# Kernel optimization log

Hardware: AMD Instinct MI355X
Metric: run time of the kernel (lower is better)

Reference implementation:

```python
import jax, jax.numpy as jnp
import numpy as np

N = 256
FEAT = 1024           # box_head.fc7.out_features
HID_REL = 256         # RelationProposalNetwork hidden_dim
GCN_HID = 256         # gcn_hidden
HEADS = 4
NUM_PARTS = 20
OUT = NUM_PARTS + 1
TOPK = 3
IN_GCN = FEAT + 4


def setup_inputs() -> dict:
    key = jax.random.key(0)
    ks = jax.random.split(key, 16)
    features = jax.random.normal(ks[0], (N, FEAT), jnp.float32)
    # valid pixel-space boxes (x1, y1, x2, y2) inside an 800x800 image
    xy = jax.random.uniform(ks[1], (N, 2), jnp.float32, 0.0, 700.0)
    wh = jax.random.uniform(ks[2], (N, 2), jnp.float32, 8.0, 100.0)
    boxes = jnp.concatenate([xy, xy + wh], axis=1)
    s = 0.02
    W_fc1 = jax.random.normal(ks[3], (2 * FEAT + 4, HID_REL), jnp.float32) * s
    b_fc1 = jnp.zeros((HID_REL,), jnp.float32)
    W_fc2 = jax.random.normal(ks[4], (HID_REL, 1), jnp.float32) * s
    b_fc2 = jnp.zeros((1,), jnp.float32)
    W1 = jax.random.normal(ks[5], (IN_GCN, HEADS * GCN_HID), jnp.float32) * s
    a_src1 = jax.random.normal(ks[6], (HEADS, GCN_HID), jnp.float32) * s
    a_dst1 = jax.random.normal(ks[7], (HEADS, GCN_HID), jnp.float32) * s
    b1 = jnp.zeros((HEADS * GCN_HID,), jnp.float32)
    W2 = jax.random.normal(ks[8], (HEADS * GCN_HID, OUT), jnp.float32) * s
    a_src2 = jax.random.normal(ks[9], (1, OUT), jnp.float32) * s
    a_dst2 = jax.random.normal(ks[10], (1, OUT), jnp.float32) * s
    b2 = jnp.zeros((OUT,), jnp.float32)
    return {
        "features": features, "boxes": boxes,
        "W_fc1": W_fc1, "b_fc1": b_fc1, "W_fc2": W_fc2, "b_fc2": b_fc2,
        "W1": W1, "a_src1": a_src1, "a_dst1": a_dst1, "b1": b1,
        "W2": W2, "a_src2": a_src2, "a_dst2": a_dst2, "b2": b2,
        "img_h": 800, "img_w": 800,
    }


def _gat_layer(x, W, a_src, a_dst, bias, s, t, n, heads, ch):
    # PyG GATConv: message flows edge_index[0] (s) -> edge_index[1] (t),
    # softmax over incoming edges of each target node t.
    h = (x @ W).reshape(n, heads, ch)                       # [n, H, C]
    e = jax.nn.leaky_relu(
        jnp.einsum("ehc,hc->eh", h[s], a_src)
        + jnp.einsum("ehc,hc->eh", h[t], a_dst), 0.2)        # [E, H]
    m = jnp.full((n, heads), -1e30, e.dtype).at[t].max(e)    # segment max
    p = jnp.exp(e - m[t])
    denom = jax.ops.segment_sum(p, t, num_segments=n)
    alpha = p / denom[t]                                     # [E, H]
    out = jax.ops.segment_sum(alpha[:, :, None] * h[s], t, num_segments=n)
    return out.reshape(n, heads * ch) + bias


def _forward(features, boxes, W_fc1, b_fc1, W_fc2, b_fc2,
             W1, a_src1, a_dst1, b1, W2, a_src2, a_dst2, b2, img_h, img_w):
    n = features.shape[0]
    # --- RelationProposalNetwork: dense O(N^2) pairwise MLP ---
    f1 = jnp.broadcast_to(features[:, None, :], (n, n, FEAT))
    f2 = jnp.broadcast_to(features[None, :, :], (n, n, FEAT))
    geom = jnp.abs(boxes[:, None, :] - boxes[None, :, :])    # [n, n, 4]
    pair = jnp.concatenate([f1, f2, geom], axis=-1)          # [n, n, 2052]
    hid = jax.nn.relu(pair @ W_fc1 + b_fc1)                  # [n, n, 256]
    rel = (hid @ W_fc2 + b_fc2)[..., 0]                      # [n, n]
    # --- top-k graph construction (drop first = self, as in source) ---
    idx = jax.lax.top_k(rel, TOPK + 1)[1][:, 1:]             # [n, topk]
    s_e = jnp.repeat(jnp.arange(n), TOPK)                    # edge_index[0]
    t_e = idx.reshape(-1)                                    # edge_index[1]
    loops = jnp.arange(n)                                    # GATConv add_self_loops
    s_e = jnp.concatenate([s_e, loops])
    t_e = jnp.concatenate([t_e, loops])
    # --- normalized box geometry node features ---
    scale = jnp.array([img_w, img_h, img_w, img_h], jnp.float32)
    nb = boxes / scale
    geomn = jnp.stack([nb[:, 0], nb[:, 1], nb[:, 2] - nb[:, 0], nb[:, 3] - nb[:, 1]], axis=1)
    gcn_in = jnp.concatenate([features, geomn], axis=1)      # [n, 1028]
    # --- AttentionalGCN: GAT(heads=4) -> ReLU -> GAT(heads=1) ---
    h1 = jax.nn.relu(_gat_layer(gcn_in, W1, a_src1, a_dst1, b1, s_e, t_e, n, HEADS, GCN_HID))
    logits = _gat_layer(h1, W2, a_src2, a_dst2, b2, s_e, t_e, n, 1, OUT)
    return logits


def reference(features, boxes, W_fc1, b_fc1, W_fc2, b_fc2,
              W1, a_src1, a_dst1, b1, W2, a_src2, a_dst2, b2, img_h, img_w):
    logits = _forward(features, boxes, W_fc1, b_fc1, W_fc2, b_fc2,
                      W1, a_src1, a_dst1, b1, W2, a_src2, a_dst2, b2, img_h, img_w)
    labels = jnp.argmax(logits, axis=1)
    return logits, labels
```

## Files before the change

kernel.cpp:

```cpp
#include <hip/hip_runtime.h>
#include <math.h>

#define NN 256
#define FEAT 1024
#define HIDR 256
#define HEADS 4
#define GCNH 256
#define M1 1024
#define OUTC 21
#define MAXDEG (NN + 1)
#define KC 8
#define KCH (FEAT / KC)
#define FCOLS 1536

__global__ __launch_bounds__(256) void k_big(
        const float* __restrict__ feat, const float* __restrict__ Wfc1,
        const float* __restrict__ W1, float* __restrict__ P) {
    __shared__ float fS[8][KCH];
    int rg = blockIdx.x, cg = blockIdx.y, kc = blockIdx.z;
    int tid = threadIdx.x;
    int r0 = rg * 8, k0 = kc * KCH;
    for (int x = tid; x < 8 * KCH; x += 256) {
        int r = x >> 7, kk = x & (KCH - 1);
        fS[r][kk] = feat[(size_t)(r0 + r) * FEAT + k0 + kk];
    }
    __syncthreads();
    int gc = cg * 512 + tid * 2;
    const float* pW;
    int ld;
    if (gc < 256)      { pW = Wfc1 + (size_t)k0 * HIDR + gc;                  ld = HIDR; }
    else if (gc < 512) { pW = Wfc1 + (size_t)(FEAT + k0) * HIDR + (gc - 256); ld = HIDR; }
    else               { pW = W1   + (size_t)k0 * M1 + (gc - 512);            ld = M1;   }
    float2 acc[8];
#pragma unroll
    for (int r = 0; r < 8; r++) { acc[r].x = 0.f; acc[r].y = 0.f; }
    for (int kk = 0; kk < KCH; kk += 4) {
        float2 w0 = *(const float2*)(pW);
        float2 w1 = *(const float2*)(pW + ld);
        float2 w2 = *(const float2*)(pW + 2 * ld);
        float2 w3 = *(const float2*)(pW + 3 * ld);
        pW += 4 * ld;
#pragma unroll
        for (int r = 0; r < 8; r++) {
            float4 f = *(const float4*)&fS[r][kk];
            acc[r].x = fmaf(f.x, w0.x, acc[r].x); acc[r].y = fmaf(f.x, w0.y, acc[r].y);
            acc[r].x = fmaf(f.y, w1.x, acc[r].x); acc[r].y = fmaf(f.y, w1.y, acc[r].y);
            acc[r].x = fmaf(f.z, w2.x, acc[r].x); acc[r].y = fmaf(f.z, w2.y, acc[r].y);
            acc[r].x = fmaf(f.w, w3.x, acc[r].x); acc[r].y = fmaf(f.w, w3.y, acc[r].y);
        }
    }
    float* Pp = P + ((size_t)kc * NN + r0) * FCOLS + gc;
#pragma unroll
    for (int r = 0; r < 8; r++)
        *(float2*)(Pp + (size_t)r * FCOLS) = acc[r];
}

__global__ __launch_bounds__(384) void k_redfix(
        const float* __restrict__ P, const float* __restrict__ bfc1,
        const float* __restrict__ boxes, const int* __restrict__ imh,
        const int* __restrict__ imw, const float* __restrict__ W1,
        const float* __restrict__ as1, const float* __restrict__ ad1,
        float* __restrict__ A, float* __restrict__ BT,
        float* __restrict__ hpre, float* __restrict__ es1,
        float* __restrict__ ed1, float* __restrict__ geomn) {
    __shared__ float gS[4];
    int row = blockIdx.x, tid = threadIdx.x;
    int c4 = tid * 4;
    const float* p = P + (size_t)row * FCOLS + c4;
    const size_t str = (size_t)NN * FCOLS;
    float4 t0 = *(const float4*)(p);
    float4 t1 = *(const float4*)(p + str);
    float4 t2 = *(const float4*)(p + 2 * str);
    float4 t3 = *(const float4*)(p + 3 * str);
    float4 t4 = *(const float4*)(p + 4 * str);
    float4 t5 = *(const float4*)(p + 5 * str);
    float4 t6 = *(const float4*)(p + 6 * str);
    float4 t7 = *(const float4*)(p + 7 * str);
    float4 s;
    s.x = ((t0.x + t1.x) + (t2.x + t3.x)) + ((t4.x + t5.x) + (t6.x + t7.x));
    s.y = ((t0.y + t1.y) + (t2.y + t3.y)) + ((t4.y + t5.y) + (t6.y + t7.y));
    s.z = ((t0.z + t1.z) + (t2.z + t3.z)) + ((t4.z + t5.z) + (t6.z + t7.z));
    s.w = ((t0.w + t1.w) + (t2.w + t3.w)) + ((t4.w + t5.w) + (t6.w + t7.w));
    if (tid == 0) {
        float w = (float)imw[0], h = (float)imh[0];
        float x1 = boxes[row * 4 + 0] / w, y1 = boxes[row * 4 + 1] / h;
        float x2 = boxes[row * 4 + 2] / w, y2 = boxes[row * 4 + 3] / h;
        gS[0] = x1; gS[1] = y1; gS[2] = x2 - x1; gS[3] = y2 - y1;
        geomn[row * 4 + 0] = x1;
        geomn[row * 4 + 1] = y1;
        geomn[row * 4 + 2] = x2 - x1;
        geomn[row * 4 + 3] = y2 - y1;
    }
    __syncthreads();
    if (c4 < 256) {
        float4 b = *(const float4*)(bfc1 + c4);
        s.x += b.x; s.y += b.y; s.z += b.z; s.w += b.w;
        *(float4*)(A + (size_t)row * HIDR + c4) = s;
    } else if (c4 < 512) {
        int kk = c4 - 256;
        BT[(kk + 0) * NN + row] = s.x;
        BT[(kk + 1) * NN + row] = s.y;
        BT[(kk + 2) * NN + row] = s.z;
        BT[(kk + 3) * NN + row] = s.w;
    } else {
        int ch = c4 - 512;
        float g0 = gS[0], g1 = gS[1], g2 = gS[2], g3 = gS[3];
        float4 wv;
        wv = *(const float4*)(W1 + (size_t)(FEAT + 0) * M1 + ch);
        s.x = fmaf(g0, wv.x, s.x); s.y = fmaf(g0, wv.y, s.y);
        s.z = fmaf(g0, wv.z, s.z); s.w = fmaf(g0, wv.w, s.w);
        wv = *(const float4*)(W1 + (size_t)(FEAT + 1) * M1 + ch);
        s.x = fmaf(g1, wv.x, s.x); s.y = fmaf(g1, wv.y, s.y);
        s.z = fmaf(g1, wv.z, s.z); s.w = fmaf(g1, wv.w, s.w);
        wv = *(const float4*)(W1 + (size_t)(FEAT + 2) * M1 + ch);
        s.x = fmaf(g2, wv.x, s.x); s.y = fmaf(g2, wv.y, s.y);
        s.z = fmaf(g2, wv.z, s.z); s.w = fmaf(g2, wv.w, s.w);
        wv = *(const float4*)(W1 + (size_t)(FEAT + 3) * M1 + ch);
        s.x = fmaf(g3, wv.x, s.x); s.y = fmaf(g3, wv.y, s.y);
        s.z = fmaf(g3, wv.z, s.z); s.w = fmaf(g3, wv.w, s.w);
        *(float4*)(hpre + (size_t)row * M1 + ch) = s;
        float4 a = *(const float4*)(as1 + ch);
        float4 b = *(const float4*)(ad1 + ch);
        float ps = s.x * a.x + s.y * a.y + s.z * a.z + s.w * a.w;
        float pd = s.x * b.x + s.y * b.y + s.z * b.z + s.w * b.w;
#pragma unroll
        for (int o = 32; o > 0; o >>= 1) {
            ps += __shfl_down(ps, o);
            pd += __shfl_down(pd, o);
        }
        if ((tid & 63) == 0) {
            int head = (tid - 128) >> 6;
            es1[row * 4 + head] = ps;
            ed1[row * 4 + head] = pd;
        }
    }
}

__global__ __launch_bounds__(512) void k_reltopk(
        const float* __restrict__ A, const float* __restrict__ BT,
        const float* __restrict__ boxes, const float* __restrict__ Wfc1,
        const float* __restrict__ Wfc2, int* __restrict__ idxTop) {
    __shared__ float As[HIDR], w2s[HIDR], wg0[HIDR], wg1[HIDR], wg2[HIDR], wg3[HIDR];
    __shared__ float sval[512];
    __shared__ unsigned long long swk[8];
    __shared__ int win;
    int i = blockIdx.x, tid = threadIdx.x;
    int j = tid & 255, half = tid >> 8;
    if (tid < 256) {
        As[tid]  = A[i * HIDR + tid];
        w2s[tid] = Wfc2[tid];
        wg0[tid] = Wfc1[(size_t)(2 * FEAT + 0) * HIDR + tid];
    } else {
        int q = tid - 256;
        wg1[q] = Wfc1[(size_t)(2 * FEAT + 1) * HIDR + q];
        wg2[q] = Wfc1[(size_t)(2 * FEAT + 2) * HIDR + q];
        wg3[q] = Wfc1[(size_t)(2 * FEAT + 3) * HIDR + q];
    }
    float bi0 = boxes[i * 4 + 0], bi1 = boxes[i * 4 + 1];
    float bi2 = boxes[i * 4 + 2], bi3 = boxes[i * 4 + 3];
    float g0 = fabsf(bi0 - boxes[j * 4 + 0]);
    float g1 = fabsf(bi1 - boxes[j * 4 + 1]);
    float g2 = fabsf(bi2 - boxes[j * 4 + 2]);
    float g3 = fabsf(bi3 - boxes[j * 4 + 3]);
    __syncthreads();
    int k0 = half * 128;
    const float* pB = BT + (size_t)k0 * NN + j;
    float acc = 0.f;
    for (int kk = k0; kk < k0 + 128; kk += 4) {
        float4 a4 = *(const float4*)&As[kk];
        float4 w4 = *(const float4*)&w2s[kk];
        float4 q0 = *(const float4*)&wg0[kk];
        float4 q1 = *(const float4*)&wg1[kk];
        float4 q2 = *(const float4*)&wg2[kk];
        float4 q3 = *(const float4*)&wg3[kk];
        float b0 = pB[0], b1 = pB[NN], b2 = pB[2 * NN], b3 = pB[3 * NN];
        pB += 4 * NN;
        float v;
        v = a4.x + b0; v = fmaf(g0, q0.x, v); v = fmaf(g1, q1.x, v);
        v = fmaf(g2, q2.x, v); v = fmaf(g3, q3.x, v);
        acc = fmaf(fmaxf(v, 0.f), w4.x, acc);
        v = a4.y + b1; v = fmaf(g0, q0.y, v); v = fmaf(g1, q1.y, v);
        v = fmaf(g2, q2.y, v); v = fmaf(g3, q3.y, v);
        acc = fmaf(fmaxf(v, 0.f), w4.y, acc);
        v = a4.z + b2; v = fmaf(g0, q0.z, v); v = fmaf(g1, q1.z, v);
        v = fmaf(g2, q2.z, v); v = fmaf(g3, q3.z, v);
        acc = fmaf(fmaxf(v, 0.f), w4.z, acc);
        v = a4.w + b3; v = fmaf(g0, q0.w, v); v = fmaf(g1, q1.w, v);
        v = fmaf(g2, q2.w, v); v = fmaf(g3, q3.w, v);
        acc = fmaf(fmaxf(v, 0.f), w4.w, acc);
    }
    sval[tid] = acc;
    __syncthreads();
    if (tid < 256) sval[tid] = sval[tid] + sval[tid + 256];
    __syncthreads();
    for (int r = 0; r < 4; r++) {
        unsigned long long key = 0ULL;
        if (tid < 256) {
            unsigned u = __float_as_uint(sval[tid]);
            u = (u & 0x80000000u) ? ~u : (u | 0x80000000u);
            key = ((unsigned long long)u << 32) | (unsigned)(NN - 1 - tid);
        }
#pragma unroll
        for (int o = 32; o > 0; o >>= 1) {
            unsigned long long nk = __shfl_down(key, o);
            if (nk > key) key = nk;
        }
        if ((tid & 63) == 0) swk[tid >> 6] = key;
        __syncthreads();
        if (tid == 0) {
            unsigned long long m = swk[0];
#pragma unroll
            for (int q = 1; q < 8; q++) if (swk[q] > m) m = swk[q];
            int wj = NN - 1 - (int)(m & 0xFFFFFFFFu);
            win = wj;
            if (r > 0) idxTop[i * 3 + (r - 1)] = wj;
        }
        __syncthreads();
        if (tid == win) sval[tid] = -1e38f;
        __syncthreads();
    }
}

__global__ __launch_bounds__(256) void k_build(
        const int* __restrict__ idxTop, int* __restrict__ deg,
        int* __restrict__ inlist) {
    __shared__ int pfx[NN];
    int t = blockIdx.x, i = threadIdx.x;
    int f = (idxTop[i * 3 + 0] == t) | (idxTop[i * 3 + 1] == t)
          | (idxTop[i * 3 + 2] == t);
    pfx[i] = f;
    __syncthreads();
    for (int o = 1; o < NN; o <<= 1) {
        int add = (i >= o) ? pfx[i - o] : 0;
        __syncthreads();
        pfx[i] += add;
        __syncthreads();
    }
    if (f) inlist[t * MAXDEG + (pfx[i] - 1)] = i;
    if (i == NN - 1) {
        int d = pfx[NN - 1];
        inlist[t * MAXDEG + d] = t;
        deg[t] = d + 1;
    }
}

__global__ __launch_bounds__(256) void k_gat1h2(
        const float* __restrict__ hpre, const float* __restrict__ es1,
        const float* __restrict__ ed1, const int* __restrict__ deg,
        const int* __restrict__ inlist, const float* __restrict__ b1,
        const float* __restrict__ W2, const float* __restrict__ as2,
        const float* __restrict__ ad2, float* __restrict__ h2,
        float* __restrict__ es2, float* __restrict__ ed2) {
    __shared__ float sc[MAXDEG * 4];
    __shared__ float mh[4], dh[4];
    __shared__ float sh[M1];
    __shared__ float part[12 * OUTC];
    __shared__ float h2row[OUTC];
    int t = blockIdx.x, tid = threadIdx.x;
    int dg = deg[t];
    for (int p = tid; p < dg * 4; p += 256) {
        int e = p >> 2, h = p & 3;
        int s = inlist[t * MAXDEG + e];
        float v = es1[s * 4 + h] + ed1[t * 4 + h];
        sc[p] = v >= 0.f ? v : 0.2f * v;
    }
    __syncthreads();
    if (tid < 4) {
        float m = -1e30f;
        for (int e = 0; e < dg; e++) m = fmaxf(m, sc[e * 4 + tid]);
        float s = 0.f;
        for (int e = 0; e < dg; e++) s += expf(sc[e * 4 + tid] - m);
        mh[tid] = m; dh[tid] = s;
    }
    __syncthreads();
    for (int p = tid; p < dg * 4; p += 256) {
        int h = p & 3;
        sc[p] = expf(sc[p] - mh[h]) / dh[h];
    }
    __syncthreads();
    float acc[4] = {0.f, 0.f, 0.f, 0.f};
    for (int e = 0; e < dg; e++) {
        int s = inlist[t * MAXDEG + e];
        const float* hs = hpre + (size_t)s * M1;
#pragma unroll
        for (int q = 0; q < 4; q++)
            acc[q] = fmaf(sc[e * 4 + q], hs[q * GCNH + tid], acc[q]);
    }
#pragma unroll
    for (int q = 0; q < 4; q++) {
        int c = q * GCNH + tid;
        sh[c] = fmaxf(acc[q] + b1[c], 0.f);
    }
    __syncthreads();
    if (tid < 252) {
        int o = tid % OUTC, p = tid / OUTC;
        float a2 = 0.f;
        for (int d = p; d < M1; d += 12)
            a2 = fmaf(sh[d], W2[d * OUTC + o], a2);
        part[p * OUTC + o] = a2;
    }
    __syncthreads();
    if (tid < OUTC) {
        float s = 0.f;
        for (int p = 0; p < 12; p++) s += part[p * OUTC + tid];
        h2[t * OUTC + tid] = s;
        h2row[tid] = s;
    }
    __syncthreads();
    if (tid == 0) {
        float s = 0.f, dd = 0.f;
        for (int k = 0; k < OUTC; k++) {
            s = fmaf(h2row[k], as2[k], s);
            dd = fmaf(h2row[k], ad2[k], dd);
        }
        es2[t] = s; ed2[t] = dd;
    }
}

__global__ __launch_bounds__(64) void k_gat2(
        const float* __restrict__ h2, const float* __restrict__ es2,
        const float* __restrict__ ed2, const int* __restrict__ deg,
        const int* __restrict__ inlist, const float* __restrict__ b2,
        float* __restrict__ out) {
    __shared__ float sc[MAXDEG];
    __shared__ float md[2];
    __shared__ float lv[OUTC];
    int t = blockIdx.x, tid = threadIdx.x;
    int dg = deg[t];
    float edt = ed2[t];
    for (int p = tid; p < dg; p += 64) {
        int s = inlist[t * MAXDEG + p];
        float v = es2[s] + edt;
        sc[p] = v >= 0.f ? v : 0.2f * v;
    }
    __syncthreads();
    if (tid == 0) {
        float m = -1e30f;
        for (int e = 0; e < dg; e++) m = fmaxf(m, sc[e]);
        float s = 0.f;
        for (int e = 0; e < dg; e++) s += expf(sc[e] - m);
        md[0] = m; md[1] = s;
    }
    __syncthreads();
    if (tid < OUTC) {
        float acc = 0.f;
        for (int e = 0; e < dg; e++) {
            int s = inlist[t * MAXDEG + e];
            float a = expf(sc[e] - md[0]) / md[1];
            acc = fmaf(a, h2[s * OUTC + tid], acc);
        }
        float v = acc + b2[tid];
        out[t * OUTC + tid] = v;
        lv[tid] = v;
    }
    __syncthreads();
    if (tid == 0) {
        int best = 0;
        float bv = lv[0];
        for (int o = 1; o < OUTC; o++)
            if (lv[o] > bv) { bv = lv[o]; best = o; }
        out[NN * OUTC + t] = (float)best;
    }
}

extern "C" void kernel_launch(void* const* d_in, const int* in_sizes, int n_in,
                              void* d_out, int out_size, void* d_ws,
                              size_t ws_size, hipStream_t stream) {
    const float* feat  = (const float*)d_in[0];
    const float* boxes = (const float*)d_in[1];
    const float* Wfc1  = (const float*)d_in[2];
    const float* bfc1  = (const float*)d_in[3];
    const float* Wfc2  = (const float*)d_in[4];
    const float* bfc2  = (const float*)d_in[5];   (void)bfc2;
    const float* W1    = (const float*)d_in[6];
    const float* as1   = (const float*)d_in[7];
    const float* ad1   = (const float*)d_in[8];
    const float* b1    = (const float*)d_in[9];
    const float* W2    = (const float*)d_in[10];
    const float* as2   = (const float*)d_in[11];
    const float* ad2   = (const float*)d_in[12];
    const float* b2    = (const float*)d_in[13];
    const int*   imh   = (const int*)d_in[14];
    const int*   imw   = (const int*)d_in[15];

    float* ws = (float*)d_ws;
    float* P     = ws;  ws += KC * NN * FCOLS;
    float* A     = ws;  ws += NN * HIDR;
    float* BT    = ws;  ws += NN * HIDR;
    float* hpre  = ws;  ws += NN * M1;
    float* es1   = ws;  ws += NN * 4;
    float* ed1   = ws;  ws += NN * 4;
    float* h2    = ws;  ws += NN * OUTC;
    float* es2   = ws;  ws += NN;
    float* ed2   = ws;  ws += NN;
    float* geomn = ws;  ws += NN * 4;
    int* deg     = (int*)ws;
    int* inlist  = deg + NN;
    int* idxTop  = inlist + NN * MAXDEG;

    float* out = (float*)d_out;

    k_big<<<dim3(32, 3, KC), 256, 0, stream>>>(feat, Wfc1, W1, P);
    k_redfix<<<NN, 384, 0, stream>>>(P, bfc1, boxes, imh, imw, W1, as1, ad1,
                                     A, BT, hpre, es1, ed1, geomn);
    k_reltopk<<<NN, 512, 0, stream>>>(A, BT, boxes, Wfc1, Wfc2, idxTop);
    k_build<<<NN, 256, 0, stream>>>(idxTop, deg, inlist);
    k_gat1h2<<<NN, 256, 0, stream>>>(hpre, es1, ed1, deg, inlist, b1,
                                     W2, as2, ad2, h2, es2, ed2);
    k_gat2<<<NN, 64, 0, stream>>>(h2, es2, ed2, deg, inlist, b2, out);
}
```

Measured before the change: 163.4 us.

## Fuse in-edge list build into GAT layer-1 kernel and retile the big GEMM

The separate k_build kernel is removed. Its prefix-scan construction of each target's incoming-edge list now runs at the start of k_gat1h2, kept in shared memory and also written out for k_gat2. This saves one kernel launch and a global round trip for the edge list. The big feature GEMM now handles 4 rows per block instead of 8, doubling the grid, and prefetches the next weight rows one iteration ahead to hide load latency. The trade-off is that each weight tile is re-read from memory twice as often.

```diff
diff --git a/kernel.cpp b/kernel.cpp
--- a/kernel.cpp
+++ b/kernel.cpp
@@ -16,11 +16,11 @@
 __global__ __launch_bounds__(256) void k_big(
         const float* __restrict__ feat, const float* __restrict__ Wfc1,
         const float* __restrict__ W1, float* __restrict__ P) {
-    __shared__ float fS[8][KCH];
+    __shared__ float fS[4][KCH];
     int rg = blockIdx.x, cg = blockIdx.y, kc = blockIdx.z;
     int tid = threadIdx.x;
-    int r0 = rg * 8, k0 = kc * KCH;
-    for (int x = tid; x < 8 * KCH; x += 256) {
+    int r0 = rg * 4, k0 = kc * KCH;
+    for (int x = tid; x < 4 * KCH; x += 256) {
         int r = x >> 7, kk = x & (KCH - 1);
         fS[r][kk] = feat[(size_t)(r0 + r) * FEAT + k0 + kk];
     }
@@ -31,27 +31,32 @@
     if (gc < 256)      { pW = Wfc1 + (size_t)k0 * HIDR + gc;                  ld = HIDR; }
     else if (gc < 512) { pW = Wfc1 + (size_t)(FEAT + k0) * HIDR + (gc - 256); ld = HIDR; }
     else               { pW = W1   + (size_t)k0 * M1 + (gc - 512);            ld = M1;   }
-    float2 acc[8];
-#pragma unroll
-    for (int r = 0; r < 8; r++) { acc[r].x = 0.f; acc[r].y = 0.f; }
+    float2 acc[4];
+#pragma unroll
+    for (int r = 0; r < 4; r++) { acc[r].x = 0.f; acc[r].y = 0.f; }
+    float2 w0 = *(const float2*)(pW);
+    float2 w1 = *(const float2*)(pW + ld);
+    float2 w2 = *(const float2*)(pW + 2 * ld);
+    float2 w3 = *(const float2*)(pW + 3 * ld);
     for (int kk = 0; kk < KCH; kk += 4) {
-        float2 w0 = *(const float2*)(pW);
-        float2 w1 = *(const float2*)(pW + ld);
-        float2 w2 = *(const float2*)(pW + 2 * ld);
-        float2 w3 = *(const float2*)(pW + 3 * ld);
         pW += 4 * ld;
-#pragma unroll
-        for (int r = 0; r < 8; r++) {
+        float2 n0 = *(const float2*)(pW);
+        float2 n1 = *(const float2*)(pW + ld);
+        float2 n2 = *(const float2*)(pW + 2 * ld);
+        float2 n3 = *(const float2*)(pW + 3 * ld);
+#pragma unroll
+        for (int r = 0; r < 4; r++) {
             float4 f = *(const float4*)&fS[r][kk];
             acc[r].x = fmaf(f.x, w0.x, acc[r].x); acc[r].y = fmaf(f.x, w0.y, acc[r].y);
             acc[r].x = fmaf(f.y, w1.x, acc[r].x); acc[r].y = fmaf(f.y, w1.y, acc[r].y);
             acc[r].x = fmaf(f.z, w2.x, acc[r].x); acc[r].y = fmaf(f.z, w2.y, acc[r].y);
             acc[r].x = fmaf(f.w, w3.x, acc[r].x); acc[r].y = fmaf(f.w, w3.y, acc[r].y);
         }
+        w0 = n0; w1 = n1; w2 = n2; w3 = n3;
     }
     float* Pp = P + ((size_t)kc * NN + r0) * FCOLS + gc;
 #pragma unroll
-    for (int r = 0; r < 8; r++)
+    for (int r = 0; r < 4; r++)
         *(float2*)(Pp + (size_t)r * FCOLS) = acc[r];
 }
 
@@ -221,46 +226,50 @@
     }
 }
 
-__global__ __launch_bounds__(256) void k_build(
-        const int* __restrict__ idxTop, int* __restrict__ deg,
-        int* __restrict__ inlist) {
+__global__ __launch_bounds__(256) void k_gat1h2(
+        const float* __restrict__ idxTopF, const float* __restrict__ hpre,
+        const float* __restrict__ es1, const float* __restrict__ ed1,
+        const float* __restrict__ b1, const float* __restrict__ W2,
+        const float* __restrict__ as2, const float* __restrict__ ad2,
+        int* __restrict__ deg, int* __restrict__ inlist,
+        float* __restrict__ h2, float* __restrict__ es2,
+        float* __restrict__ ed2) {
+    const int* idxTop = (const int*)idxTopF;
     __shared__ int pfx[NN];
-    int t = blockIdx.x, i = threadIdx.x;
-    int f = (idxTop[i * 3 + 0] == t) | (idxTop[i * 3 + 1] == t)
-          | (idxTop[i * 3 + 2] == t);
-    pfx[i] = f;
-    __syncthreads();
-    for (int o = 1; o < NN; o <<= 1) {
-        int add = (i >= o) ? pfx[i - o] : 0;
-        __syncthreads();
-        pfx[i] += add;
-        __syncthreads();
-    }
-    if (f) inlist[t * MAXDEG + (pfx[i] - 1)] = i;
-    if (i == NN - 1) {
-        int d = pfx[NN - 1];
-        inlist[t * MAXDEG + d] = t;
-        deg[t] = d + 1;
-    }
-}
-
-__global__ __launch_bounds__(256) void k_gat1h2(
-        const float* __restrict__ hpre, const float* __restrict__ es1,
-        const float* __restrict__ ed1, const int* __restrict__ deg,
-        const int* __restrict__ inlist, const float* __restrict__ b1,
-        const float* __restrict__ W2, const float* __restrict__ as2,
-        const float* __restrict__ ad2, float* __restrict__ h2,
-        float* __restrict__ es2, float* __restrict__ ed2) {
+    __shared__ int lst[MAXDEG];
+    __shared__ int dgS;
     __shared__ float sc[MAXDEG * 4];
     __shared__ float mh[4], dh[4];
     __shared__ float sh[M1];
     __shared__ float part[12 * OUTC];
     __shared__ float h2row[OUTC];
     int t = blockIdx.x, tid = threadIdx.x;
-    int dg = deg[t];
+    int f = (idxTop[tid * 3 + 0] == t) | (idxTop[tid * 3 + 1] == t)
+          | (idxTop[tid * 3 + 2] == t);
+    pfx[tid] = f;
+    __syncthreads();
+    for (int o = 1; o < NN; o <<= 1) {
+        int add = (tid >= o) ? pfx[tid - o] : 0;
+        __syncthreads();
+        pfx[tid] += add;
+        __syncthreads();
+    }
+    if (f) {
+        lst[pfx[tid] - 1] = tid;
+        inlist[t * MAXDEG + (pfx[tid] - 1)] = tid;
+    }
+    if (tid == NN - 1) {
+        int d = pfx[NN - 1];
+        lst[d] = t;
+        inlist[t * MAXDEG + d] = t;
+        dgS = d + 1;
+        deg[t] = d + 1;
+    }
+    __syncthreads();
+    int dg = dgS;
     for (int p = tid; p < dg * 4; p += 256) {
         int e = p >> 2, h = p & 3;
-        int s = inlist[t * MAXDEG + e];
+        int s = lst[e];
         float v = es1[s * 4 + h] + ed1[t * 4 + h];
         sc[p] = v >= 0.f ? v : 0.2f * v;
     }
@@ -280,7 +289,7 @@
     __syncthreads();
     float acc[4] = {0.f, 0.f, 0.f, 0.f};
     for (int e = 0; e < dg; e++) {
-        int s = inlist[t * MAXDEG + e];
+        int s = lst[e];
         const float* hs = hpre + (size_t)s * M1;
 #pragma unroll
         for (int q = 0; q < 4; q++)
@@ -400,12 +409,12 @@
 
     float* out = (float*)d_out;
 
-    k_big<<<dim3(32, 3, KC), 256, 0, stream>>>(feat, Wfc1, W1, P);
+    k_big<<<dim3(64, 3, KC), 256, 0, stream>>>(feat, Wfc1, W1, P);
     k_redfix<<<NN, 384, 0, stream>>>(P, bfc1, boxes, imh, imw, W1, as1, ad1,
                                      A, BT, hpre, es1, ed1, geomn);
     k_reltopk<<<NN, 512, 0, stream>>>(A, BT, boxes, Wfc1, Wfc2, idxTop);
-    k_build<<<NN, 256, 0, stream>>>(idxTop, deg, inlist);
-    k_gat1h2<<<NN, 256, 0, stream>>>(hpre, es1, ed1, deg, inlist, b1,
-                                     W2, as2, ad2, h2, es2, ed2);
+    k_gat1h2<<<NN, 256, 0, stream>>>((const float*)idxTop, hpre, es1, ed1,
+                                     b1, W2, as2, ad2, deg, inlist,
+                                     h2, es2, ed2);
     k_gat2<<<NN, 64, 0, stream>>>(h2, es2, ed2, deg, inlist, b2, out);
 }
```

After: 171.1 us. 1.05x slower.
